# Optimization experiments

Hardware: AMD Instinct MI355X
Metric: run time of the kernel (lower is better)

Reference implementation:

```python
import jax, jax.numpy as jnp
import numpy as np

MARGIN = 0.2
NEG_INF = -1e30


def setup_inputs() -> dict:
    key = jax.random.key(0)
    k1, k2 = jax.random.split(key)
    B, D, C = 384, 256, 48
    features = jax.random.normal(k1, (B, D), dtype=jnp.float32)
    labels = jax.random.randint(k2, (B,), 0, C, dtype=jnp.int32)
    return {"features": features, "labels": labels, "epoch": 5}


def reference(features, labels, epoch):
    B = features.shape[0]
    # pairwise euclidean distance, clamped like torch.clamp(min=1e-11)
    diff = features[:, None, :] - features[None, :, :]          # [B,B,D]
    dist = jnp.sqrt(jnp.clip(jnp.sum(diff * diff, axis=-1), 1e-11))  # [B,B]

    idx = jnp.arange(B)
    same = labels[:, None] == labels[None, :]
    pos_mask = same & (idx[None, :] > idx[:, None])             # pairs (i,j), j>i, same label
    neg_mask = ~same

    # Gumbel-max sampling replaces the per-row np.random.choice host loop.
    gumbel = jax.random.gumbel(jax.random.key(42), (B, B, B), dtype=dist.dtype)

    if epoch > 3:
        # semi-hard negatives: pos_dist < d(i,k) < pos_dist + margin, weights 1/d(i,k)
        d_ik = dist[:, None, :]                                 # [B,1,B]
        d_pos = dist[:, :, None]                                # [B,B,1]
        semi = neg_mask[:, None, :] & (d_ik > d_pos) & (d_ik < d_pos + MARGIN)  # [B,B,B]
        logits = jnp.where(semi, -jnp.log(dist)[:, None, :], NEG_INF)  # log(1/d)
        has_neg = jnp.any(semi, axis=-1)                        # [B,B]
    else:
        # uniform random negative per (i,j) pair
        logits = jnp.where(neg_mask[:, None, :], 0.0, NEG_INF)  # [B,1,B]
        has_neg = jnp.broadcast_to(jnp.any(neg_mask, axis=-1)[:, None], (B, B))

    neg_idx = jnp.argmax(logits + gumbel, axis=-1)              # [B,B]
    neg_dist = jnp.take_along_axis(dist, neg_idx, axis=1)       # d(i, sampled_neg)

    valid = pos_mask & has_neg
    # MarginRankingLoss(neg, pos, target=1) = relu(pos - neg + margin)
    per_pair = jax.nn.relu(dist - neg_dist + MARGIN)
    count = jnp.sum(valid)
    total = jnp.sum(jnp.where(valid, per_pair, 0.0))
    return jnp.where(count > 0, total / jnp.maximum(count, 1), 0.0)
```

## Files before the change

kernel.cpp:

```cpp
#include <hip/hip_runtime.h>
#include <hip/hip_bf16.h>
#include <stdint.h>

#define BSZ 384
#define DD  256
#define NBLK 256
#define NDUAL (BSZ - NBLK)
#define NWAVES 6
#define NEG_BIG -3.0e38f
#define DONE_BASE 0xAAAAAAAAu

__device__ __forceinline__ void threefry_0_42(uint32_t c0, uint32_t c1,
                                              uint32_t& o0, uint32_t& o1) {
    const uint32_t k0 = 0u;
    const uint32_t k1 = 42u;
    const uint32_t k2 = 0u ^ 42u ^ 0x1BD11BDAu;
    uint32_t x0 = c0 + k0;
    uint32_t x1 = c1 + k1;
#define TF_RND(R) { x0 += x1; x1 = (x1 << (R)) | (x1 >> (32 - (R))); x1 ^= x0; }
    TF_RND(13) TF_RND(15) TF_RND(26) TF_RND(6)
    x0 += k1; x1 += k2 + 1u;
    TF_RND(17) TF_RND(29) TF_RND(16) TF_RND(24)
    x0 += k2; x1 += k0 + 2u;
    TF_RND(13) TF_RND(15) TF_RND(26) TF_RND(6)
    x0 += k0; x1 += k1 + 3u;
    TF_RND(17) TF_RND(29) TF_RND(16) TF_RND(24)
    x0 += k1; x1 += k2 + 4u;
    TF_RND(13) TF_RND(15) TF_RND(26) TF_RND(6)
    x0 += k2; x1 += k0 + 5u;
#undef TF_RND
    o0 = x0; o1 = x1;
}

__device__ __forceinline__ float gumbel_at(uint32_t idx) {
    uint32_t r0, r1;
    threefry_0_42(0u, idx, r0, r1);
    uint32_t bits = r0 ^ r1;
    uint32_t mant = bits >> 9;
    float f = __uint_as_float(mant | 0x3F800000u) - 1.0f;
    float u = (mant == 0u) ? 1.17549435e-38f : f;
    return -logf(-logf(u));
}

__global__ __launch_bounds__(BSZ) void fused_kernel(const float* __restrict__ F,
                                                    const int* __restrict__ labels,
                                                    const int* __restrict__ epochp,
                                                    float* __restrict__ tot_slot,
                                                    unsigned int* __restrict__ cnt_slot,
                                                    unsigned int* __restrict__ done,
                                                    float* __restrict__ out) {
    __shared__ float    row[2][BSZ];
    __shared__ float    nlg[2][BSZ];
    __shared__ int      slab[BSZ];
    __shared__ int      plist[512];
    __shared__ int      npos;
    __shared__ int      is_last;
    __shared__ float    wtot[NWAVES];
    __shared__ unsigned wcnt[NWAVES];

    const int b    = blockIdx.x;
    const int tid  = threadIdx.x;
    const int wave = tid >> 6;
    const int lane = tid & 63;
    const int rl   = lane >> 3;
    const int s    = lane & 7;

    const int  i0   = b;
    const bool dual = (b < NDUAL);
    const int  i1   = dual ? (NBLK + b) : 0;

    slab[tid] = labels[tid];
    if (tid == 0) npos = 0;
    __syncthreads();

    const int lab0 = slab[i0];
    const int lab1 = dual ? slab[i1] : -1;
    if (tid > i0 && slab[tid] == lab0)
        plist[atomicAdd(&npos, 1)] = tid;
    if (dual && tid > i1 && slab[tid] == lab1)
        plist[atomicAdd(&npos, 1)] = 512 | tid;
    const int  epoch   = *epochp;
    const bool semisel = (epoch > 3);
    __syncthreads();

    const int np = npos;
    float    t_total = 0.0f;
    unsigned t_count = 0u;

    if (np > 0) {
        const float4* F4 = (const float4*)F;

        float4 f0[8], f1[8];
#pragma unroll
        for (int t = 0; t < 8; ++t) f0[t] = F4[i0 * (DD / 4) + t * 8 + s];
        if (dual) {
#pragma unroll
            for (int t = 0; t < 8; ++t) f1[t] = F4[i1 * (DD / 4) + t * 8 + s];
        }

        if (dual) {
            for (int c = 0; c < 8; ++c) {
                const int k = c * 48 + wave * 8 + rl;
                const float4* fk = F4 + (size_t)k * (DD / 4);
                float a0 = 0.f, a1 = 0.f, a2 = 0.f, a3 = 0.f;
                float b0 = 0.f, b1 = 0.f, b2 = 0.f, b3 = 0.f;
#pragma unroll
                for (int t = 0; t < 8; ++t) {
                    float4 bb = fk[t * 8 + s];
                    float d0 = f0[t].x - bb.x;
                    float d1 = f0[t].y - bb.y;
                    float d2 = f0[t].z - bb.z;
                    float d3 = f0[t].w - bb.w;
                    a0 = fmaf(d0, d0, a0);
                    a1 = fmaf(d1, d1, a1);
                    a2 = fmaf(d2, d2, a2);
                    a3 = fmaf(d3, d3, a3);
                    float e0 = f1[t].x - bb.x;
                    float e1 = f1[t].y - bb.y;
                    float e2 = f1[t].z - bb.z;
                    float e3 = f1[t].w - bb.w;
                    b0 = fmaf(e0, e0, b0);
                    b1 = fmaf(e1, e1, b1);
                    b2 = fmaf(e2, e2, b2);
                    b3 = fmaf(e3, e3, b3);
                }
                float p = (a0 + a1) + (a2 + a3);
                p += __shfl_down(p, 4, 64);
                p += __shfl_down(p, 2, 64);
                p += __shfl_down(p, 1, 64);
                if (s == 0) row[0][k] = sqrtf(fmaxf(p, 1e-11f));
                float q = (b0 + b1) + (b2 + b3);
                q += __shfl_down(q, 4, 64);
                q += __shfl_down(q, 2, 64);
                q += __shfl_down(q, 1, 64);
                if (s == 0) row[1][k] = sqrtf(fmaxf(q, 1e-11f));
            }
        } else {
            for (int c = 0; c < 8; ++c) {
                const int k = c * 48 + wave * 8 + rl;
                const float4* fk = F4 + (size_t)k * (DD / 4);
                float a0 = 0.f, a1 = 0.f, a2 = 0.f, a3 = 0.f;
#pragma unroll
                for (int t = 0; t < 8; ++t) {
                    float4 bb = fk[t * 8 + s];
                    float d0 = f0[t].x - bb.x;
                    float d1 = f0[t].y - bb.y;
                    float d2 = f0[t].z - bb.z;
                    float d3 = f0[t].w - bb.w;
                    a0 = fmaf(d0, d0, a0);
                    a1 = fmaf(d1, d1, a1);
                    a2 = fmaf(d2, d2, a2);
                    a3 = fmaf(d3, d3, a3);
                }
                float p = (a0 + a1) + (a2 + a3);
                p += __shfl_down(p, 4, 64);
                p += __shfl_down(p, 2, 64);
                p += __shfl_down(p, 1, 64);
                if (s == 0) row[0][k] = sqrtf(fmaxf(p, 1e-11f));
            }
        }
        __syncthreads();
        nlg[0][tid] = semisel ? -logf(row[0][tid]) : 0.0f;
        if (dual) nlg[1][tid] = semisel ? -logf(row[1][tid]) : 0.0f;
        __syncthreads();

        for (int p = wave; p < np; p += NWAVES) {
            const int   e     = plist[p];
            const int   a     = e >> 9;
            const int   j     = e & 511;
            const int   ia    = a ? i1 : i0;
            const int   laba  = a ? lab1 : lab0;
            const float d_pos = row[a][j];
            const float hi    = d_pos + 0.2f;
            float v  = NEG_BIG;
            int   kk = 0;
#pragma unroll
            for (int c = 0; c < BSZ / 64; ++c) {
                const int   k   = c * 64 + lane;
                const float dkk = row[a][k];
                const bool cand = (slab[k] != laba) &&
                                  (!semisel || (dkk > d_pos && dkk < hi));
                if (__any(cand)) {
                    if (cand) {
                        const uint32_t idx = (uint32_t)(ia * BSZ + j) * (uint32_t)BSZ
                                             + (uint32_t)k;
                        float val = nlg[a][k] + gumbel_at(idx);
                        if (val > v) { v = val; kk = k; }
                    }
                }
            }
#pragma unroll
            for (int off = 32; off; off >>= 1) {
                float ov = __shfl_down(v, off, 64);
                int   oi = __shfl_down(kk, off, 64);
                if (ov > v || (ov == v && oi < kk)) { v = ov; kk = oi; }
            }
            if (lane == 0 && v > -1.0e38f) {
                t_total += fmaxf(d_pos - row[a][kk] + 0.2f, 0.0f);
                t_count += 1u;
            }
        }
    }

    if (lane == 0) { wtot[wave] = t_total; wcnt[wave] = t_count; }
    __syncthreads();
    if (tid == 0) {
        float    tt = 0.0f;
        unsigned cc = 0u;
#pragma unroll
        for (int q = 0; q < NWAVES; ++q) { tt += wtot[q]; cc += wcnt[q]; }
        atomicExch(&tot_slot[b], tt);
        atomicExch(&cnt_slot[b], cc);
        __threadfence();
        const unsigned prev = atomicAdd(done, 1u);
        is_last = (prev == DONE_BASE + (unsigned)(NBLK - 1)) ? 1 : 0;
    }
    __syncthreads();

    if (is_last) {
        float    t = (tid < NBLK) ? atomicAdd(&tot_slot[tid], 0.0f) : 0.0f;
        unsigned c = (tid < NBLK) ? atomicAdd(&cnt_slot[tid], 0u)  : 0u;
#pragma unroll
        for (int off = 32; off; off >>= 1) {
            t += __shfl_down(t, off, 64);
            c += __shfl_down(c, off, 64);
        }
        if (lane == 0) { wtot[wave] = t; wcnt[wave] = c; }
        __syncthreads();
        if (tid == 0) {
            float    tt = 0.0f;
            unsigned cc = 0u;
#pragma unroll
            for (int q = 0; q < NWAVES; ++q) { tt += wtot[q]; cc += wcnt[q]; }
            out[0] = (cc > 0u) ? (tt / (float)cc) : 0.0f;
        }
    }
}

extern "C" void kernel_launch(void* const* d_in, const int* in_sizes, int n_in,
                              void* d_out, int out_size, void* d_ws, size_t ws_size,
                              hipStream_t stream) {
    const float* F      = (const float*)d_in[0];
    const int*   labels = (const int*)d_in[1];
    const int*   epoch  = (const int*)d_in[2];
    float*       out    = (float*)d_out;

    if (ws_size < (2 * NBLK + 1) * sizeof(float)) return;
    float*        tot_slot = (float*)d_ws;
    unsigned int* cnt_slot = (unsigned int*)d_ws + NBLK;
    unsigned int* done     = (unsigned int*)d_ws + 2 * NBLK;

    fused_kernel<<<NBLK, BSZ, 0, stream>>>(F, labels, epoch,
                                           tot_slot, cnt_slot, done, out);
}
```

Before: 78.07 us.

## Double block width to 768 threads and stage anchor rows in shared memory

Launches 768 threads (12 waves) per block instead of 384, so the distance loop takes 4 iterations per wave instead of 8 and the sampling loop spreads positive pairs over twice as many waves. Anchor feature vectors now go into LDS once instead of living in per-thread registers, which frees registers to allow the larger block and more waves per CU. The cost is an LDS read of the anchor per inner step and extra guards for threads beyond index 384.

```diff
diff --git a/kernel.cpp b/kernel.cpp
--- a/kernel.cpp
+++ b/kernel.cpp
@@ -6,7 +6,8 @@
 #define DD  256
 #define NBLK 256
 #define NDUAL (BSZ - NBLK)
-#define NWAVES 6
+#define NTHR 768
+#define NWAVES 12
 #define NEG_BIG -3.0e38f
 #define DONE_BASE 0xAAAAAAAAu
 
@@ -42,15 +43,16 @@
     return -logf(-logf(u));
 }
 
-__global__ __launch_bounds__(BSZ) void fused_kernel(const float* __restrict__ F,
-                                                    const int* __restrict__ labels,
-                                                    const int* __restrict__ epochp,
-                                                    float* __restrict__ tot_slot,
-                                                    unsigned int* __restrict__ cnt_slot,
-                                                    unsigned int* __restrict__ done,
-                                                    float* __restrict__ out) {
+__global__ __launch_bounds__(NTHR, 4) void fused_kernel(const float* __restrict__ F,
+                                                        const int* __restrict__ labels,
+                                                        const int* __restrict__ epochp,
+                                                        float* __restrict__ tot_slot,
+                                                        unsigned int* __restrict__ cnt_slot,
+                                                        unsigned int* __restrict__ done,
+                                                        float* __restrict__ out) {
     __shared__ float    row[2][BSZ];
     __shared__ float    nlg[2][BSZ];
+    __shared__ float4   anc[2][DD/4];
     __shared__ int      slab[BSZ];
     __shared__ int      plist[512];
     __shared__ int      npos;
@@ -67,18 +69,24 @@
 
     const int  i0   = b;
     const bool dual = (b < NDUAL);
-    const int  i1   = dual ? (NBLK + b) : 0;
-
-    slab[tid] = labels[tid];
+    const int  i1   = NBLK + b;
+
+    const float4* F4 = (const float4*)F;
+
+    if (tid < BSZ) slab[tid] = labels[tid];
     if (tid == 0) npos = 0;
+    if (tid < DD / 4)                 anc[0][tid]          = F4[i0 * (DD / 4) + tid];
+    else if (dual && tid < 2 * (DD / 4)) anc[1][tid - DD/4] = F4[i1 * (DD / 4) + (tid - DD/4)];
     __syncthreads();
 
     const int lab0 = slab[i0];
     const int lab1 = dual ? slab[i1] : -1;
-    if (tid > i0 && slab[tid] == lab0)
-        plist[atomicAdd(&npos, 1)] = tid;
-    if (dual && tid > i1 && slab[tid] == lab1)
-        plist[atomicAdd(&npos, 1)] = 512 | tid;
+    if (tid < BSZ) {
+        if (tid > i0 && slab[tid] == lab0)
+            plist[atomicAdd(&npos, 1)] = tid;
+        if (dual && tid > i1 && slab[tid] == lab1)
+            plist[atomicAdd(&npos, 1)] = 512 | tid;
+    }
     const int  epoch   = *epochp;
     const bool semisel = (epoch > 3);
     __syncthreads();
@@ -88,37 +96,29 @@
     unsigned t_count = 0u;
 
     if (np > 0) {
-        const float4* F4 = (const float4*)F;
-
-        float4 f0[8], f1[8];
-#pragma unroll
-        for (int t = 0; t < 8; ++t) f0[t] = F4[i0 * (DD / 4) + t * 8 + s];
         if (dual) {
-#pragma unroll
-            for (int t = 0; t < 8; ++t) f1[t] = F4[i1 * (DD / 4) + t * 8 + s];
-        }
-
-        if (dual) {
-            for (int c = 0; c < 8; ++c) {
-                const int k = c * 48 + wave * 8 + rl;
+            for (int c = 0; c < 4; ++c) {
+                const int k = c * 96 + wave * 8 + rl;
                 const float4* fk = F4 + (size_t)k * (DD / 4);
                 float a0 = 0.f, a1 = 0.f, a2 = 0.f, a3 = 0.f;
                 float b0 = 0.f, b1 = 0.f, b2 = 0.f, b3 = 0.f;
 #pragma unroll
                 for (int t = 0; t < 8; ++t) {
                     float4 bb = fk[t * 8 + s];
-                    float d0 = f0[t].x - bb.x;
-                    float d1 = f0[t].y - bb.y;
-                    float d2 = f0[t].z - bb.z;
-                    float d3 = f0[t].w - bb.w;
+                    float4 f0 = anc[0][t * 8 + s];
+                    float4 f1 = anc[1][t * 8 + s];
+                    float d0 = f0.x - bb.x;
+                    float d1 = f0.y - bb.y;
+                    float d2 = f0.z - bb.z;
+                    float d3 = f0.w - bb.w;
                     a0 = fmaf(d0, d0, a0);
                     a1 = fmaf(d1, d1, a1);
                     a2 = fmaf(d2, d2, a2);
                     a3 = fmaf(d3, d3, a3);
-                    float e0 = f1[t].x - bb.x;
-                    float e1 = f1[t].y - bb.y;
-                    float e2 = f1[t].z - bb.z;
-                    float e3 = f1[t].w - bb.w;
+                    float e0 = f1.x - bb.x;
+                    float e1 = f1.y - bb.y;
+                    float e2 = f1.z - bb.z;
+                    float e3 = f1.w - bb.w;
                     b0 = fmaf(e0, e0, b0);
                     b1 = fmaf(e1, e1, b1);
                     b2 = fmaf(e2, e2, b2);
@@ -136,17 +136,18 @@
                 if (s == 0) row[1][k] = sqrtf(fmaxf(q, 1e-11f));
             }
         } else {
-            for (int c = 0; c < 8; ++c) {
-                const int k = c * 48 + wave * 8 + rl;
+            for (int c = 0; c < 4; ++c) {
+                const int k = c * 96 + wave * 8 + rl;
                 const float4* fk = F4 + (size_t)k * (DD / 4);
                 float a0 = 0.f, a1 = 0.f, a2 = 0.f, a3 = 0.f;
 #pragma unroll
                 for (int t = 0; t < 8; ++t) {
                     float4 bb = fk[t * 8 + s];
-                    float d0 = f0[t].x - bb.x;
-                    float d1 = f0[t].y - bb.y;
-                    float d2 = f0[t].z - bb.z;
-                    float d3 = f0[t].w - bb.w;
+                    float4 f0 = anc[0][t * 8 + s];
+                    float d0 = f0.x - bb.x;
+                    float d1 = f0.y - bb.y;
+                    float d2 = f0.z - bb.z;
+                    float d3 = f0.w - bb.w;
                     a0 = fmaf(d0, d0, a0);
                     a1 = fmaf(d1, d1, a1);
                     a2 = fmaf(d2, d2, a2);
@@ -160,8 +161,8 @@
             }
         }
         __syncthreads();
-        nlg[0][tid] = semisel ? -logf(row[0][tid]) : 0.0f;
-        if (dual) nlg[1][tid] = semisel ? -logf(row[1][tid]) : 0.0f;
+        if (tid < BSZ)       nlg[0][tid]       = semisel ? -logf(row[0][tid])       : 0.0f;
+        else if (dual)       nlg[1][tid - BSZ] = semisel ? -logf(row[1][tid - BSZ]) : 0.0f;
         __syncthreads();
 
         for (int p = wave; p < np; p += NWAVES) {
@@ -218,8 +219,12 @@
     __syncthreads();
 
     if (is_last) {
-        float    t = (tid < NBLK) ? atomicAdd(&tot_slot[tid], 0.0f) : 0.0f;
-        unsigned c = (tid < NBLK) ? atomicAdd(&cnt_slot[tid], 0u)  : 0u;
+        float    t = 0.0f;
+        unsigned c = 0u;
+        if (tid < NBLK) {
+            t = atomicAdd(&tot_slot[tid], 0.0f);
+            c = atomicAdd(&cnt_slot[tid], 0u);
+        }
 #pragma unroll
         for (int off = 32; off; off >>= 1) {
             t += __shfl_down(t, off, 64);
@@ -250,6 +255,6 @@
     unsigned int* cnt_slot = (unsigned int*)d_ws + NBLK;
     unsigned int* done     = (unsigned int*)d_ws + 2 * NBLK;
 
-    fused_kernel<<<NBLK, BSZ, 0, stream>>>(F, labels, epoch,
-                                           tot_slot, cnt_slot, done, out);
-}
+    fused_kernel<<<NBLK, NTHR, 0, stream>>>(F, labels, epoch,
+                                            tot_slot, cnt_slot, done, out);
+}
```

New measurement: 69.32 us. 11.2% less time.
